# Kernel tuning notes

Measured on AMD Instinct MI355X. Metric: run time of the kernel, lower is better.

## Reference

```python
import jax, jax.numpy as jnp
import numpy as np

B, IN_DIM, HID, ODE_STEPS = 8192, 1024, 1024, 6
DT = 1.0


def setup_inputs() -> dict:
    key = jax.random.key(0)
    ks = jax.random.split(key, 8)
    s = 0.02  # init scale for stability
    return {
        "x": jax.random.normal(ks[0], (B, IN_DIM), dtype=jnp.float32),
        "h": jax.random.normal(ks[1], (B, HID), dtype=jnp.float32),
        "log_tau": jnp.zeros((HID,), dtype=jnp.float32),
        "W_in_w": jax.random.normal(ks[2], (HID, IN_DIM), dtype=jnp.float32) * s,
        "W_in_b": jnp.zeros((HID,), dtype=jnp.float32),
        "W_rec_w": jax.random.normal(ks[3], (HID, HID), dtype=jnp.float32) * s,
        "W_gate_w": jax.random.normal(ks[4], (HID, IN_DIM + HID), dtype=jnp.float32) * s,
        "W_gate_b": jnp.zeros((HID,), dtype=jnp.float32),
    }


def reference(x, h, log_tau, W_in_w, W_in_b, W_rec_w, W_gate_w, W_gate_b):
    # torch Linear: y = x @ W.T + b, W:(out,in)
    tau = jnp.exp(log_tau)                      # (HID,)
    input_drive = x @ W_in_w.T + W_in_b         # (B,HID), loop-invariant
    # W_gate acts on concat([x, h]); split into x-block and h-block.
    Wg_x = W_gate_w[:, :IN_DIM]
    Wg_h = W_gate_w[:, IN_DIM:]
    gate_x = x @ Wg_x.T + W_gate_b              # (B,HID), loop-invariant
    sub_dt = DT / ODE_STEPS
    scale = sub_dt / tau                        # (HID,)

    def step(h, _):
        gate = jax.nn.sigmoid(gate_x + h @ Wg_h.T)
        f = -h + gate * jnp.tanh(input_drive + h @ W_rec_w.T)
        return h + scale * f, None

    h, _ = jax.lax.scan(step, h, None, length=ODE_STEPS)
    return (h, h)
```

## Files before the change

### kernel.cpp

```cpp
#include <hip/hip_runtime.h>
#include <hip/hip_bf16.h>
#include <stdint.h>

#define B_DIM 8192
#define IN_DIMC 1024
#define HIDC 1024
#define K_DIM 1024
#define ODE_STEPS 6

typedef float f32x4 __attribute__((ext_vector_type(4)));
typedef short bf16x8 __attribute__((ext_vector_type(8)));
typedef unsigned short u16x8 __attribute__((ext_vector_type(8)));

__device__ __forceinline__ float bf2f(unsigned short u) {
    union { unsigned int u; float f; } c; c.u = ((unsigned int)u) << 16; return c.f;
}
__device__ __forceinline__ unsigned short f2bf(float f) {
    union { float f; unsigned int u; } c; c.f = f;
    unsigned int u = c.u;
    return (unsigned short)((u + 0x7fffu + ((u >> 16) & 1u)) >> 16);
}
__device__ __forceinline__ float fast_tanh(float x) {
    float e = __expf(2.0f * x);
    return 1.0f - 2.0f / (e + 1.0f);
}

constexpr size_t XN    = (size_t)B_DIM * IN_DIMC;
constexpr size_t HN    = (size_t)B_DIM * HIDC;
constexpr size_t WINN  = (size_t)HIDC * IN_DIMC;
constexpr size_t WRECN = (size_t)HIDC * HIDC;
constexpr size_t WGN   = (size_t)HIDC * (IN_DIMC + HIDC);
constexpr size_t TOTQ  = (XN + HN + WINN + WRECN + WGN) / 4;

__global__ __launch_bounds__(256) void convert_all(
    const float* __restrict__ x, const float* __restrict__ h,
    const float* __restrict__ win, const float* __restrict__ wrec,
    const float* __restrict__ wgate,
    unsigned short* __restrict__ x_bf, unsigned short* __restrict__ h_bf,
    unsigned short* __restrict__ win_bf, unsigned short* __restrict__ wrec_bf,
    unsigned short* __restrict__ wgx_bf, unsigned short* __restrict__ wgh_bf)
{
    size_t q = (size_t)blockIdx.x * 256 + threadIdx.x;
    if (q >= TOTQ) return;
    size_t e = q * 4;
    const float* src; unsigned short* dst; size_t si, di;
    if (e < XN)                          { src = x;    si = e;                       dst = x_bf;    di = si; }
    else if (e < XN + HN)                { src = h;    si = e - XN;                  dst = h_bf;    di = si; }
    else if (e < XN + HN + WINN)         { src = win;  si = e - XN - HN;             dst = win_bf;  di = si; }
    else if (e < XN + HN + WINN + WRECN) { src = wrec; si = e - XN - HN - WINN;      dst = wrec_bf; di = si; }
    else {
        size_t i = e - XN - HN - WINN - WRECN;
        size_t row = i >> 11, col = i & 2047;
        src = wgate; si = i;
        if (col < 1024) { dst = wgx_bf; di = row * 1024 + col; }
        else            { dst = wgh_bf; di = row * 1024 + (col - 1024); }
    }
    float4 v = *(const float4*)(src + si);
    ushort4 o;
    o.x = f2bf(v.x); o.y = f2bf(v.y); o.z = f2bf(v.z); o.w = f2bf(v.w);
    *(ushort4*)(dst + di) = o;
}

constexpr int BM = 128, BN = 64, BK = 32;
constexpr int NT = HIDC / BN;

__device__ __forceinline__ void gload_lds16(const void* g, void* l) {
    __builtin_amdgcn_global_load_lds(
        (const __attribute__((address_space(1))) void*)g,
        (__attribute__((address_space(3))) void*)l, 16, 0, 0);
}

template<bool STEP>
__global__ __launch_bounds__(256, 3) void ltc_gemm(
    const unsigned short* __restrict__ A,
    const unsigned short* __restrict__ B1,
    const unsigned short* __restrict__ B2,
    const unsigned short* __restrict__ GXID,
    const float* __restrict__ h_init,
    float* __restrict__ h_nat,
    const float* __restrict__ log_tau,
    float* __restrict__ h_out,
    float* __restrict__ h_out2,
    unsigned short* __restrict__ hbf_out,
    const float* __restrict__ bias1, const float* __restrict__ bias2,
    unsigned short* __restrict__ GXID_out)
{
    __shared__ __attribute__((aligned(16))) unsigned short lA[BM * BK];
    __shared__ __attribute__((aligned(16))) unsigned short lB1[BN * BK];
    __shared__ __attribute__((aligned(16))) unsigned short lB2[BN * BK];

    const int tid = threadIdx.x;
    const int w = tid >> 6, l = tid & 63;
    const int mt = blockIdx.x / NT, nt = blockIdx.x % NT;
    const int m0 = mt * BM, n0 = nt * BN;
    const int wm = (w >> 1) * 64, wn = (w & 1) * 32;
    const int lrow = l >> 2, lcol = (l & 3) * 8;
    const int lm = l & 15, lq = l >> 4;

    f32x4 acc1[4][2], acc2[4][2];
    f32x4 z4 = {0.f, 0.f, 0.f, 0.f};
    #pragma unroll
    for (int i = 0; i < 4; i++)
        #pragma unroll
        for (int j = 0; j < 2; j++) { acc1[i][j] = z4; acc2[i][j] = z4; }

    const int arow = w * 32;
    const unsigned short* Bsrc = (w < 2) ? B1 : B2;
    unsigned short* lBdst = (w < 2) ? lB1 : lB2;
    const int brow = (w & 1) * 32;

    for (int k0 = 0; k0 < K_DIM; k0 += BK) {
        #pragma unroll
        for (int i = 0; i < 2; i++) {
            int ra = arow + i * 16;
            int rb = brow + i * 16;
            gload_lds16(A    + (size_t)(m0 + ra + lrow) * K_DIM + k0 + lcol, &lA[ra * BK]);
            gload_lds16(Bsrc + (size_t)(n0 + rb + lrow) * K_DIM + k0 + lcol, &lBdst[rb * BK]);
        }
        __syncthreads();

        bf16x8 af[4], f1[2], f2[2];
        #pragma unroll
        for (int mi = 0; mi < 4; mi++)
            af[mi] = *(const bf16x8*)&lA[(wm + mi * 16 + lm) * BK + lq * 8];
        #pragma unroll
        for (int ni = 0; ni < 2; ni++) {
            f1[ni] = *(const bf16x8*)&lB1[(wn + ni * 16 + lm) * BK + lq * 8];
            f2[ni] = *(const bf16x8*)&lB2[(wn + ni * 16 + lm) * BK + lq * 8];
        }
        #pragma unroll
        for (int mi = 0; mi < 4; mi++)
            #pragma unroll
            for (int ni = 0; ni < 2; ni++) {
                acc1[mi][ni] = __builtin_amdgcn_mfma_f32_16x16x32_bf16(af[mi], f1[ni], acc1[mi][ni], 0, 0, 0);
                acc2[mi][ni] = __builtin_amdgcn_mfma_f32_16x16x32_bf16(af[mi], f2[ni], acc2[mi][ni], 0, 0, 0);
            }
        __syncthreads();
    }

    constexpr float subdt = 1.0f / (float)ODE_STEPS;
    const size_t wslot = (((size_t)blockIdx.x * 4 + w) * 8) * 64 + l;

    #pragma unroll
    for (int mi = 0; mi < 4; mi++) {
        #pragma unroll
        for (int ni = 0; ni < 2; ni++) {
            const int gmb = m0 + wm + mi * 16 + lq * 4;
            const int gn  = n0 + wn + ni * 16 + lm;
            const size_t slot = wslot + (size_t)(mi * 2 + ni) * 64;
            if (STEP) {
                const float sc = subdt * __expf(-log_tau[gn]);
                u16x8 gi = *(const u16x8*)&GXID[slot * 8];
                f32x4 st;
                if (h_init) {
                    #pragma unroll
                    for (int r = 0; r < 4; r++)
                        st[r] = h_init[(size_t)(gmb + r) * HIDC + gn];
                } else {
                    st = *(const f32x4*)&h_nat[slot * 4];
                }
                f32x4 hn;
                #pragma unroll
                for (int r = 0; r < 4; r++) {
                    float gx = bf2f((unsigned short)gi[r])     + acc1[mi][ni][r];
                    float dr = bf2f((unsigned short)gi[4 + r]) + acc2[mi][ni][r];
                    float gt = fast_tanh(dr) / (1.0f + __expf(-gx));
                    hn[r] = fmaf(sc, gt - st[r], st[r]);
                }
                if (h_out) {
                    #pragma unroll
                    for (int r = 0; r < 4; r++) {
                        size_t idx = (size_t)(gmb + r) * HIDC + gn;
                        h_out[idx]  = hn[r];
                        h_out2[idx] = hn[r];
                    }
                } else {
                    *(f32x4*)&h_nat[slot * 4] = hn;
                    #pragma unroll
                    for (int r = 0; r < 4; r++)
                        hbf_out[(size_t)(gmb + r) * HIDC + gn] = f2bf(hn[r]);
                }
            } else {
                const float b1 = bias1[gn], b2 = bias2[gn];
                u16x8 o;
                #pragma unroll
                for (int r = 0; r < 4; r++) {
                    o[r]     = f2bf(acc1[mi][ni][r] + b1);
                    o[4 + r] = f2bf(acc2[mi][ni][r] + b2);
                }
                *(u16x8*)&GXID_out[slot * 8] = o;
            }
        }
    }
}

extern "C" void kernel_launch(void* const* d_in, const int* in_sizes, int n_in,
                              void* d_out, int out_size, void* d_ws, size_t ws_size,
                              hipStream_t stream)
{
    const float* x    = (const float*)d_in[0];
    const float* h    = (const float*)d_in[1];
    const float* ltau = (const float*)d_in[2];
    const float* winw = (const float*)d_in[3];
    const float* winb = (const float*)d_in[4];
    const float* wrec = (const float*)d_in[5];
    const float* wg   = (const float*)d_in[6];
    const float* wgb  = (const float*)d_in[7];

    char* ws = (char*)d_ws;
    unsigned short* x_bf    = (unsigned short*)ws; ws += XN * 2;
    unsigned short* h_bf0   = (unsigned short*)ws; ws += HN * 2;
    unsigned short* h_bf1   = (unsigned short*)ws; ws += HN * 2;
    unsigned short* win_bf  = (unsigned short*)ws; ws += WINN * 2;
    unsigned short* wrec_bf = (unsigned short*)ws; ws += WRECN * 2;
    unsigned short* wgx_bf  = (unsigned short*)ws; ws += WINN * 2;
    unsigned short* wgh_bf  = (unsigned short*)ws; ws += WRECN * 2;
    unsigned short* GXID    = (unsigned short*)ws; ws += HN * 2 * 2;
    float*          h_nat   = (float*)ws;          ws += HN * 4;

    float* hout  = (float*)d_out;
    float* hout2 = hout + (size_t)B_DIM * HIDC;

    convert_all<<<(int)(TOTQ / 256), 256, 0, stream>>>(
        x, h, winw, wrec, wg, x_bf, h_bf0, win_bf, wrec_bf, wgx_bf, wgh_bf);

    const int grid = (B_DIM / BM) * NT;
    ltc_gemm<false><<<grid, 256, 0, stream>>>(
        x_bf, wgx_bf, win_bf,
        nullptr, nullptr, nullptr, nullptr, nullptr, nullptr, nullptr,
        wgb, winb, GXID);

    unsigned short* hbf[2] = {h_bf0, h_bf1};
    for (int s = 0; s < ODE_STEPS; s++) {
        const bool last = (s == ODE_STEPS - 1);
        ltc_gemm<true><<<grid, 256, 0, stream>>>(
            hbf[s & 1], wgh_bf, wrec_bf,
            GXID,
            (s == 0) ? h : nullptr,
            h_nat, ltau,
            last ? hout : nullptr, last ? hout2 : nullptr,
            last ? nullptr : hbf[(s + 1) & 1],
            nullptr, nullptr, nullptr);
    }
}
```

Measured before the change: 521.1 us.

## Reuse bf16 h tile from LDS for state update instead of fp32 h_nat

```diff
diff --git a/kernel.cpp b/kernel.cpp
--- a/kernel.cpp
+++ b/kernel.cpp
@@ -76,8 +76,6 @@
     const unsigned short* __restrict__ B1,
     const unsigned short* __restrict__ B2,
     const unsigned short* __restrict__ GXID,
-    const float* __restrict__ h_init,
-    float* __restrict__ h_nat,
     const float* __restrict__ log_tau,
     float* __restrict__ h_out,
     float* __restrict__ h_out2,
@@ -88,6 +86,7 @@
     __shared__ __attribute__((aligned(16))) unsigned short lA[BM * BK];
     __shared__ __attribute__((aligned(16))) unsigned short lB1[BN * BK];
     __shared__ __attribute__((aligned(16))) unsigned short lB2[BN * BK];
+    __shared__ __attribute__((aligned(16))) unsigned short lH[BM * BK];
 
     const int tid = threadIdx.x;
     const int w = tid >> 6, l = tid & 63;
@@ -97,6 +96,27 @@
     const int lrow = l >> 2, lcol = (l & 3) * 8;
     const int lm = l & 15, lq = l >> 4;
 
+    const size_t wslot = (((size_t)blockIdx.x * 4 + w) * 8) * 64 + l;
+
+    u16x8 gi[4][2];
+    float sc[2], bb1[2], bb2[2];
+    #pragma unroll
+    for (int ni = 0; ni < 2; ni++) {
+        const int gn = n0 + wn + ni * 16 + lm;
+        if (STEP) {
+            sc[ni] = (1.0f / (float)ODE_STEPS) * __expf(-log_tau[gn]);
+        } else {
+            bb1[ni] = bias1[gn]; bb2[ni] = bias2[gn];
+        }
+    }
+    if (STEP) {
+        #pragma unroll
+        for (int mi = 0; mi < 4; mi++)
+            #pragma unroll
+            for (int ni = 0; ni < 2; ni++)
+                gi[mi][ni] = *(const u16x8*)&GXID[(wslot + (size_t)(mi * 2 + ni) * 64) * 8];
+    }
+
     f32x4 acc1[4][2], acc2[4][2];
     f32x4 z4 = {0.f, 0.f, 0.f, 0.f};
     #pragma unroll
@@ -109,15 +129,23 @@
     unsigned short* lBdst = (w < 2) ? lB1 : lB2;
     const int brow = (w & 1) * 32;
 
-    for (int k0 = 0; k0 < K_DIM; k0 += BK) {
-        #pragma unroll
-        for (int i = 0; i < 2; i++) {
-            int ra = arow + i * 16;
-            int rb = brow + i * 16;
+    for (int i = 0; i < 32; i++) {
+        const int k0 = (n0 + 64 + i * 32) & (K_DIM - 1);
+        #pragma unroll
+        for (int j = 0; j < 2; j++) {
+            int ra = arow + j * 16;
+            int rb = brow + j * 16;
             gload_lds16(A    + (size_t)(m0 + ra + lrow) * K_DIM + k0 + lcol, &lA[ra * BK]);
             gload_lds16(Bsrc + (size_t)(n0 + rb + lrow) * K_DIM + k0 + lcol, &lBdst[rb * BK]);
         }
         __syncthreads();
+
+        if (STEP && i == 30) {
+            const bf16x8* s = (const bf16x8*)lA;
+            bf16x8* d = (bf16x8*)lH;
+            d[tid] = s[tid];
+            d[tid + 256] = s[tid + 256];
+        }
 
         bf16x8 af[4], f1[2], f2[2];
         #pragma unroll
@@ -138,34 +166,25 @@
         __syncthreads();
     }
 
-    constexpr float subdt = 1.0f / (float)ODE_STEPS;
-    const size_t wslot = (((size_t)blockIdx.x * 4 + w) * 8) * 64 + l;
-
     #pragma unroll
     for (int mi = 0; mi < 4; mi++) {
         #pragma unroll
         for (int ni = 0; ni < 2; ni++) {
             const int gmb = m0 + wm + mi * 16 + lq * 4;
             const int gn  = n0 + wn + ni * 16 + lm;
-            const size_t slot = wslot + (size_t)(mi * 2 + ni) * 64;
             if (STEP) {
-                const float sc = subdt * __expf(-log_tau[gn]);
-                u16x8 gi = *(const u16x8*)&GXID[slot * 8];
-                f32x4 st;
-                if (h_init) {
-                    #pragma unroll
-                    for (int r = 0; r < 4; r++)
-                        st[r] = h_init[(size_t)(gmb + r) * HIDC + gn];
-                } else {
-                    st = *(const f32x4*)&h_nat[slot * 4];
-                }
+                const int cl = wn + ni * 16 + lm;
+                const unsigned short* hsrc = (cl < 32) ? lH : lA;
+                const int cc = cl & 31;
                 f32x4 hn;
                 #pragma unroll
                 for (int r = 0; r < 4; r++) {
-                    float gx = bf2f((unsigned short)gi[r])     + acc1[mi][ni][r];
-                    float dr = bf2f((unsigned short)gi[4 + r]) + acc2[mi][ni][r];
+                    const int rl = wm + mi * 16 + lq * 4 + r;
+                    float hv = bf2f(hsrc[rl * BK + cc]);
+                    float gx = bf2f((unsigned short)gi[mi][ni][r])     + acc1[mi][ni][r];
+                    float dr = bf2f((unsigned short)gi[mi][ni][4 + r]) + acc2[mi][ni][r];
                     float gt = fast_tanh(dr) / (1.0f + __expf(-gx));
-                    hn[r] = fmaf(sc, gt - st[r], st[r]);
+                    hn[r] = fmaf(sc[ni], gt - hv, hv);
                 }
                 if (h_out) {
                     #pragma unroll
@@ -175,20 +194,18 @@
                         h_out2[idx] = hn[r];
                     }
                 } else {
-                    *(f32x4*)&h_nat[slot * 4] = hn;
                     #pragma unroll
                     for (int r = 0; r < 4; r++)
                         hbf_out[(size_t)(gmb + r) * HIDC + gn] = f2bf(hn[r]);
                 }
             } else {
-                const float b1 = bias1[gn], b2 = bias2[gn];
                 u16x8 o;
                 #pragma unroll
                 for (int r = 0; r < 4; r++) {
-                    o[r]     = f2bf(acc1[mi][ni][r] + b1);
-                    o[4 + r] = f2bf(acc2[mi][ni][r] + b2);
+                    o[r]     = f2bf(acc1[mi][ni][r] + bb1[ni]);
+                    o[4 + r] = f2bf(acc2[mi][ni][r] + bb2[ni]);
                 }
-                *(u16x8*)&GXID_out[slot * 8] = o;
+                *(u16x8*)&GXID_out[(wslot + (size_t)(mi * 2 + ni) * 64) * 8] = o;
             }
         }
     }
@@ -216,7 +233,6 @@
     unsigned short* wgx_bf  = (unsigned short*)ws; ws += WINN * 2;
     unsigned short* wgh_bf  = (unsigned short*)ws; ws += WRECN * 2;
     unsigned short* GXID    = (unsigned short*)ws; ws += HN * 2 * 2;
-    float*          h_nat   = (float*)ws;          ws += HN * 4;
 
     float* hout  = (float*)d_out;
     float* hout2 = hout + (size_t)B_DIM * HIDC;
@@ -227,7 +243,7 @@
     const int grid = (B_DIM / BM) * NT;
     ltc_gemm<false><<<grid, 256, 0, stream>>>(
         x_bf, wgx_bf, win_bf,
-        nullptr, nullptr, nullptr, nullptr, nullptr, nullptr, nullptr,
+        nullptr, nullptr, nullptr, nullptr, nullptr,
         wgb, winb, GXID);
 
     unsigned short* hbf[2] = {h_bf0, h_bf1};
@@ -235,9 +251,7 @@
         const bool last = (s == ODE_STEPS - 1);
         ltc_gemm<true><<<grid, 256, 0, stream>>>(
             hbf[s & 1], wgh_bf, wrec_bf,
-            GXID,
-            (s == 0) ? h : nullptr,
-            h_nat, ltau,
+            GXID, ltau,
             last ? hout : nullptr, last ? hout2 : nullptr,
             last ? nullptr : hbf[(s + 1) & 1],
             nullptr, nullptr, nullptr);
```

New measurement: 558.2 us. 7.1% more time.
